# Performance work log

Hardware: AMD Instinct MI355X
Metric: run time of the kernel (lower is better)

The kernel has to match this reference:

```python
import jax, jax.numpy as jnp
import numpy as np

B, S, D, E = 8, 2048, 1024, 8
TOKENS = B * S
CAPACITY = TOKENS // E  # capacity_factor=1.0, top-1 gating (deepspeed default)


def _moe_layer(x_flat, Wg, We, be):
    """DeepSpeed-style top-1 MoE: gate -> capacity drop -> dispatch -> expert GEMM -> combine.
    x_flat: [T, D]; Wg: [D, E]; We: [E, D, D]; be: [E, D]."""
    gates = jax.nn.softmax(x_flat @ Wg, axis=-1)              # [T, E]
    idx = jnp.argmax(gates, axis=1)                            # [T] expert per token
    mask = jax.nn.one_hot(idx, E, dtype=jnp.int32)             # [T, E]
    loc = jnp.cumsum(mask, axis=0) - 1                         # position within expert
    loc_s = jnp.sum(loc * mask, axis=1)                        # [T]
    keep = loc_s < CAPACITY                                    # capacity drop
    gate_s = jnp.sum(gates * mask.astype(gates.dtype), axis=1) * keep.astype(gates.dtype)
    slot = jnp.clip(loc_s, 0, CAPACITY - 1)
    # dispatch: scatter kept tokens into [E, C, D] buffer (slots are unique for kept tokens)
    disp = jnp.zeros((E, CAPACITY, D), x_flat.dtype).at[idx, slot].add(
        x_flat * keep[:, None].astype(x_flat.dtype))
    # grouped expert GEMM
    eo = jnp.einsum('ecd,edf->ecf', disp, We) + be[:, None, :]  # [E, C, D]
    # combine: gather each token's expert output, scale by its gate value
    return eo[idx, slot] * gate_s[:, None]                      # [T, D]


def reference(x, y, W1, b1, Wg2, We2, be2, Wg3, We3, be3):
    h = jnp.einsum('bsd,df->bsf', x, W1) + b1                  # dense pre-layer
    hf = h.reshape(TOKENS, D)
    o = _moe_layer(hf, Wg2, We2, be2)
    o = _moe_layer(o, Wg3, We3, be3)
    h = h + o.reshape(B, S, D)                                 # residual add
    sent = h.mean(axis=1)                                      # [B, D]
    logp = jax.nn.log_softmax(sent, axis=-1)
    return -jnp.mean(logp[jnp.arange(B), y])                   # CrossEntropyLoss


def setup_inputs() -> dict:
    key = jax.random.key(0)
    ks = jax.random.split(key, 10)
    s = 0.02
    return {
        'x': jax.random.normal(ks[0], (B, S, D), jnp.float32),
        'y': jax.random.randint(ks[1], (B,), 0, D),
        'W1': jax.random.normal(ks[2], (D, D), jnp.float32) * s,
        'b1': jnp.zeros((D,), jnp.float32),
        'Wg2': jax.random.normal(ks[3], (D, E), jnp.float32) * s,
        'We2': jax.random.normal(ks[4], (E, D, D), jnp.float32) * s,
        'be2': jnp.zeros((E, D), jnp.float32),
        'Wg3': jax.random.normal(ks[5], (D, E), jnp.float32) * s,
        'We3': jax.random.normal(ks[6], (E, D, D), jnp.float32) * s,
        'be3': jnp.zeros((E, D), jnp.float32),
    }
```

## Files before the change

### kernel.cpp

```cpp
#include <hip/hip_runtime.h>
#include <hip/hip_bf16.h>
#include <math.h>


#define TOKS 16384
#define DIM 1024
#define NEXP 8
#define CAP 2048
#define BATCH 8
#define SEQ 2048

typedef __bf16 bf16_t;
typedef __bf16 bf16x8 __attribute__((ext_vector_type(8)));
typedef float fx4 __attribute__((ext_vector_type(4)));

__device__ __forceinline__ void gll16(const bf16_t* g, bf16_t* l) {
  __builtin_amdgcn_global_load_lds(
      (const __attribute__((address_space(1))) unsigned int*)g,
      (__attribute__((address_space(3))) unsigned int*)l, 16, 0, 0);
}

#define BARRIER() asm volatile("s_barrier" ::: "memory")
#define LGKM0()   asm volatile("s_waitcnt lgkmcnt(0)" ::: "memory")
#define VMC(N)    asm volatile("s_waitcnt vmcnt(" #N ")" ::: "memory")

#define PW_BLOCKS (17 * 64)
__global__ __launch_bounds__(256) void k_prep_w(
    const float* __restrict__ W1, const float* __restrict__ We2,
    const float* __restrict__ We3, bf16_t* __restrict__ Wt) {
  __shared__ bf16_t T[256][68];
  const int id = blockIdx.x;
  const int tid = threadIdx.x;
  const int m = id >> 6, rem = id & 63;
  const int k0 = (rem >> 4) * 256, n0 = (rem & 15) * 64;
  const float* src = (m == 0) ? W1
                     : (m <= 8) ? We2 + (size_t)(m - 1) * DIM * DIM
                                : We3 + (size_t)(m - 9) * DIM * DIM;
  bf16_t* dst = Wt + (size_t)m * DIM * DIM;
  const int r = tid >> 4, nq = tid & 15;
#pragma unroll
  for (int i = 0; i < 16; i++) {
    const int k = i * 16 + r;
    float4 v = *(const float4*)&src[(size_t)(k0 + k) * DIM + n0 + nq * 4];
    union { bf16_t h[4]; uint2 u; } t;
    t.h[0] = (bf16_t)v.x; t.h[1] = (bf16_t)v.y;
    t.h[2] = (bf16_t)v.z; t.h[3] = (bf16_t)v.w;
    *(uint2*)&T[k][(nq ^ ((k >> 3) & 15)) << 2] = t.u;
  }
  __syncthreads();
#pragma unroll
  for (int p = 0; p < 8; p++) {
    const int idx2 = p * 256 + tid;
    const int nl = idx2 >> 5, ks = (idx2 & 31) * 8;
    union { bf16_t h[8]; uint4 u; } o;
#pragma unroll
    for (int j = 0; j < 8; j++) {
      const int k = ks + j;
      o.h[j] = T[k][((((nl >> 2) ^ ((k >> 3) & 15)) << 2) | (nl & 3))];
    }
    *(uint4*)&dst[(size_t)(n0 + nl) * DIM + k0 + ks] = o.u;
  }
}

#define CVT_BLOCKS (TOKS * DIM / 8 / 256)
#define PREPX_GRID (2 + CVT_BLOCKS + 1)
__global__ __launch_bounds__(256) void k_prep_x(
    const float* __restrict__ Wg2, const float* __restrict__ Wg3,
    const float* __restrict__ x, bf16_t* __restrict__ WgP,
    bf16_t* __restrict__ xb, uint4* __restrict__ zreg, int znq) {
  const int id = blockIdx.x;
  const int tid = threadIdx.x;
  if (id < 2) {
    const int which = id;
    const float* src = which ? Wg3 : Wg2;
    bf16_t* dst = WgP + which * (128 * 8 * 8);
#pragma unroll
    for (int j = 0; j < 4; j++) {
      int d = tid * 4 + j;
      float4 a = *(const float4*)&src[d * 8];
      float4 b = *(const float4*)&src[d * 8 + 4];
      float v[8] = {a.x, a.y, a.z, a.w, b.x, b.y, b.z, b.w};
#pragma unroll
      for (int e = 0; e < 8; e++)
        dst[((d >> 3) * 8 + e) * 8 + (d & 7)] = (bf16_t)v[e];
    }
  } else if (id < 2 + CVT_BLOCKS) {
    const int cid = id - 2;
    size_t i = ((size_t)cid * 256 + tid) * 8;
    float4 a = *(const float4*)&x[i];
    float4 b = *(const float4*)&x[i + 4];
    union { bf16_t h[8]; uint4 u; } t;
    t.h[0] = (bf16_t)a.x; t.h[1] = (bf16_t)a.y; t.h[2] = (bf16_t)a.z; t.h[3] = (bf16_t)a.w;
    t.h[4] = (bf16_t)b.x; t.h[5] = (bf16_t)b.y; t.h[6] = (bf16_t)b.z; t.h[7] = (bf16_t)b.w;
    *(uint4*)&xb[i] = t.u;
  } else {
    const uint4 z = {0u, 0u, 0u, 0u};
    for (int i = tid; i < znq; i += 256) zreg[i] = z;
  }
}

template <int MODE>
__global__ __launch_bounds__(512) void k_gemm256(
    const bf16_t* __restrict__ A, const bf16_t* __restrict__ Bt0,
    const float* __restrict__ bias0, bf16_t* __restrict__ out,
    float* __restrict__ sent, const int* __restrict__ tok,
    const int* __restrict__ cnt, const float* __restrict__ gate,
    const bf16_t* __restrict__ zp, float* __restrict__ slabs) {
  __shared__ alignas(16) bf16_t As[2][256 * 64];
  __shared__ alignas(16) bf16_t Bs[2][256 * 64];
  const int tid = threadIdx.x;
  const int lane = tid & 63, wave = tid >> 6;
  const int quad = lane >> 4, l15 = lane & 15;
  const int wm = wave >> 2, wn = wave & 3;
  const int id = blockIdx.x;
  const int xcd = id & 7, rem = id >> 3;
  const int n0 = (rem & 3) * 256;

  int m0;
  int count = 0;
  const bf16_t* Bt;
  const float* bias;
  const int* tk = nullptr;
  if constexpr (MODE == 0) {
    m0 = (xcd * 8 + (rem >> 2)) * 256;
    Bt = Bt0;
    bias = bias0;
  } else {
    m0 = (rem >> 2) * 256;
    count = cnt[xcd];
    if (m0 >= count) {
      if constexpr (MODE == 2) {
        float* slab = slabs + (size_t)id * 2048;
        for (int i = tid; i < 2048; i += 512) slab[i] = 0.f;
      }
      return;
    }
    Bt = Bt0 + (size_t)xcd * DIM * DIM;
    bias = bias0 + xcd * DIM;
    tk = tok + xcd * CAP;
  }

  const int kc = (tid & 7) ^ ((tid >> 3) & 7);
  const int rbase = tid >> 3;

  const bf16_t* gA[4];
  const bf16_t* gB[4];
#pragma unroll
  for (int h = 0; h < 2; h++)
#pragma unroll
    for (int i = 0; i < 2; i++) {
      const int r = h * 128 + i * 64 + rbase;
      if constexpr (MODE == 0) {
        gA[h * 2 + i] = A + (size_t)(m0 + r) * DIM + kc * 8;
      } else {
        const int ca = m0 + r;
        gA[h * 2 + i] = (ca < count) ? A + (size_t)tk[ca] * DIM + kc * 8 : zp;
      }
      gB[h * 2 + i] = Bt + (size_t)(n0 + r) * DIM + kc * 8;
    }

  auto stA = [&](int t, int half) {
#pragma unroll
    for (int i = 0; i < 2; i++)
      gll16(gA[half * 2 + i] + t * 64,
            &As[t & 1][(half * 128 + i * 64 + wave * 8) * 64]);
  };
  auto stB = [&](int t, int half) {
#pragma unroll
    for (int i = 0; i < 2; i++)
      gll16(gB[half * 2 + i] + t * 64,
            &Bs[t & 1][(half * 128 + i * 64 + wave * 8) * 64]);
  };
  auto rdA = [&](bf16x8 (&av)[4][2], int buf, int mh) {
#pragma unroll
    for (int mf = 0; mf < 4; mf++)
#pragma unroll
      for (int s = 0; s < 2; s++)
        av[mf][s] = *(const bf16x8*)&As[buf][(wm * 128 + (mh * 4 + mf) * 16 + l15) * 64 +
                                            (((s * 4 + quad) ^ (l15 & 7)) << 3)];
  };
  auto rdB = [&](bf16x8 (&bv)[2][2], int buf, int nh) {
#pragma unroll
    for (int nf = 0; nf < 2; nf++)
#pragma unroll
      for (int s = 0; s < 2; s++)
        bv[nf][s] = *(const bf16x8*)&Bs[buf][(wn * 64 + (nh * 2 + nf) * 16 + l15) * 64 +
                                            (((s * 4 + quad) ^ (l15 & 7)) << 3)];
  };

  fx4 acc[8][4];
#pragma unroll
  for (int i = 0; i < 8; i++)
#pragma unroll
    for (int j = 0; j < 4; j++) acc[i][j] = (fx4)0.0f;

  auto mma = [&](bf16x8 (&av)[4][2], bf16x8 (&bv)[2][2], int mh, int nh) {
    __builtin_amdgcn_s_setprio(1);
#pragma unroll
    for (int s = 0; s < 2; s++)
#pragma unroll
      for (int mf = 0; mf < 4; mf++)
#pragma unroll
        for (int nf = 0; nf < 2; nf++)
          acc[mh * 4 + mf][nh * 2 + nf] = __builtin_amdgcn_mfma_f32_16x16x32_bf16(
              av[mf][s], bv[nf][s], acc[mh * 4 + mf][nh * 2 + nf], 0, 0, 0);
    __builtin_amdgcn_s_setprio(0);
  };

  stA(0, 0); stA(0, 1); stB(0, 0); stB(0, 1);
  stB(1, 0); stB(1, 1); stA(1, 0);
  VMC(6);
  BARRIER();

  bf16x8 av0[4][2], av1[4][2], bv0[2][2], bv1[2][2];
#pragma unroll 2
  for (int t = 0; t < 14; t++) {
    const int buf = t & 1;
    rdA(av0, buf, 0); rdB(bv0, buf, 0); rdB(bv1, buf, 1);
    stA(t + 1, 1);
    BARRIER(); LGKM0();
    mma(av0, bv0, 0, 0);
    BARRIER();
    stB(t + 2, 0);
    BARRIER();
    mma(av0, bv1, 0, 1);
    BARRIER();
    rdA(av1, buf, 1);
    stB(t + 2, 1);
    BARRIER(); LGKM0();
    mma(av1, bv1, 1, 1);
    BARRIER();
    stA(t + 2, 0);
    mma(av1, bv0, 1, 0);
    VMC(6);
    BARRIER();
  }
  {
    rdA(av0, 0, 0); rdB(bv0, 0, 0); rdB(bv1, 0, 1);
    stA(15, 1);
    BARRIER(); LGKM0();
    mma(av0, bv0, 0, 0);
    BARRIER();
    mma(av0, bv1, 0, 1);
    BARRIER();
    rdA(av1, 0, 1);
    BARRIER(); LGKM0();
    mma(av1, bv1, 1, 1);
    BARRIER();
    mma(av1, bv0, 1, 0);
    VMC(0);
    BARRIER();
  }
  {
    rdA(av0, 1, 0); rdB(bv0, 1, 0); rdB(bv1, 1, 1); rdA(av1, 1, 1);
    LGKM0();
    mma(av0, bv0, 0, 0); mma(av0, bv1, 0, 1);
    mma(av1, bv1, 1, 1); mma(av1, bv0, 1, 0);
  }

  float bb[4];
#pragma unroll
  for (int nf = 0; nf < 4; nf++) bb[nf] = bias[n0 + wn * 64 + nf * 16 + l15];
  if constexpr (MODE == 0) {
    float sj[4] = {0.f, 0.f, 0.f, 0.f};
#pragma unroll
    for (int mf = 0; mf < 8; mf++)
#pragma unroll
      for (int r = 0; r < 4; r++) {
        const int rowL = wm * 128 + mf * 16 + quad * 4 + r;
#pragma unroll
        for (int nf = 0; nf < 4; nf++) {
          const float v = acc[mf][nf][r] + bb[nf];
          sj[nf] += v;
          out[(size_t)(m0 + rowL) * DIM + n0 + wn * 64 + nf * 16 + l15] = (bf16_t)v;
        }
      }
#pragma unroll
    for (int nf = 0; nf < 4; nf++) {
      sj[nf] += __shfl_xor(sj[nf], 16);
      sj[nf] += __shfl_xor(sj[nf], 32);
    }
    if (quad == 0)
#pragma unroll
      for (int nf = 0; nf < 4; nf++)
        atomicAdd(&sent[(m0 >> 11) * DIM + n0 + wn * 64 + nf * 16 + l15],
                  sj[nf] * (1.0f / SEQ));
  } else if constexpr (MODE == 1) {
#pragma unroll
    for (int mf = 0; mf < 8; mf++)
#pragma unroll
      for (int r = 0; r < 4; r++) {
        const int c = m0 + wm * 128 + mf * 16 + quad * 4 + r;
        if (c < count) {
          const int tkn = tk[c];
          const float g = gate[tkn];
#pragma unroll
          for (int nf = 0; nf < 4; nf++)
            out[(size_t)tkn * DIM + n0 + wn * 64 + nf * 16 + l15] =
                (bf16_t)((acc[mf][nf][r] + bb[nf]) * g);
        }
      }
  } else {
    float colacc[4][8];
#pragma unroll
    for (int nf = 0; nf < 4; nf++)
#pragma unroll
      for (int b2 = 0; b2 < 8; b2++) colacc[nf][b2] = 0.f;
#pragma unroll
    for (int mf = 0; mf < 8; mf++)
#pragma unroll
      for (int r = 0; r < 4; r++) {
        const int c = m0 + wm * 128 + mf * 16 + quad * 4 + r;
        if (c < count) {
          const int tkn = tk[c];
          const float g = gate[tkn];
          const int b = tkn >> 11;
#pragma unroll
          for (int nf = 0; nf < 4; nf++) {
            const float v = (acc[mf][nf][r] + bb[nf]) * g;
#pragma unroll
            for (int b2 = 0; b2 < 8; b2++)
              colacc[nf][b2] += (b == b2) ? v : 0.f;
          }
        }
      }
#pragma unroll
    for (int nf = 0; nf < 4; nf++)
#pragma unroll
      for (int b2 = 0; b2 < 8; b2++) {
        colacc[nf][b2] += __shfl_xor(colacc[nf][b2], 16);
        colacc[nf][b2] += __shfl_xor(colacc[nf][b2], 32);
      }
    __syncthreads();
    float* swm = (float*)&As[0][0];
    if (quad == 0) {
#pragma unroll
      for (int nf = 0; nf < 4; nf++)
#pragma unroll
        for (int b2 = 0; b2 < 8; b2++)
          swm[(wm * 8 + b2) * 256 + wn * 64 + nf * 16 + l15] = colacc[nf][b2];
    }
    __syncthreads();
    float* slab = slabs + (size_t)id * 2048;
    for (int i = tid; i < 2048; i += 512)
      slab[i] = swm[i] + swm[2048 + i];
  }
}

__global__ __launch_bounds__(256) void k_gate_mm(
    const bf16_t* __restrict__ act, const bf16_t* __restrict__ WgPx,
    int* __restrict__ idx, float* __restrict__ gate) {
  __shared__ alignas(16) bf16_t As[64 * 64];
  __shared__ alignas(16) bf16_t WgS[128 * 64];
  __shared__ float L[64][8];
  const int tid = threadIdx.x;
  const int lane = tid & 63, wave = tid >> 6;
  const int quad = lane >> 4, l15 = lane & 15;
  const int m0 = blockIdx.x * 64;
  const int kc = (tid & 7) ^ ((tid >> 3) & 7);
  const int rbase = tid >> 3;

#pragma unroll
  for (int j = 0; j < 4; j++)
    gll16(WgPx + (j * 256 + wave * 64 + lane) * 8, &WgS[(j * 256 + wave * 64) * 8]);

  const bf16_t* gA[2]; bf16_t* lA[2];
#pragma unroll
  for (int i = 0; i < 2; i++) {
    gA[i] = act + (size_t)(m0 + rbase + 32 * i) * DIM + kc * 8;
    lA[i] = &As[wave * 512 + i * 2048];
  }
  fx4 acc = (fx4)0.0f;
  for (int k0 = 0; k0 < DIM; k0 += 64) {
#pragma unroll
    for (int i = 0; i < 2; i++) gll16(gA[i] + k0, lA[i]);
    __syncthreads();
#pragma unroll
    for (int s = 0; s < 2; s++) {
      const int pofs = ((s * 4 + quad) ^ (l15 & 7)) << 3;
      bf16x8 av = *(const bf16x8*)&As[(wave * 16 + l15) * 64 + pofs];
      bf16x8 bv = *(const bf16x8*)&WgS[((k0 >> 3) + s * 4 + quad) * 64 + (l15 & 7) * 8];
      acc = __builtin_amdgcn_mfma_f32_16x16x32_bf16(av, bv, acc, 0, 0, 0);
    }
    __syncthreads();
  }
  if (l15 < 8) {
#pragma unroll
    for (int r = 0; r < 4; r++) L[wave * 16 + quad * 4 + r][l15] = acc[r];
  }
  __syncthreads();
  if (tid < 64) {
    float lg[8];
#pragma unroll
    for (int e = 0; e < 8; e++) lg[e] = L[tid][e];
    float best = lg[0];
    int bi = 0;
#pragma unroll
    for (int e = 1; e < 8; e++)
      if (lg[e] > best) { best = lg[e]; bi = e; }
    float s = 0.f;
#pragma unroll
    for (int e = 0; e < 8; e++) s += expf(lg[e] - best);
    idx[m0 + tid] = bi;
    gate[m0 + tid] = 1.0f / s;
  }
}

#define DLMAX 2048
__global__ __launch_bounds__(1024) void k_route(
    const int* __restrict__ idx, int* __restrict__ tok, int* __restrict__ cnt,
    bf16_t* __restrict__ obuf) {
  const int e = blockIdx.x;
  const int tid = threadIdx.x, lane = tid & 63, wv = tid >> 6;
  __shared__ int wsum[16];
  __shared__ int dlist[DLMAX];
  const int4* p = (const int4*)(idx + tid * 16);
  int m[16];
  int c = 0;
#pragma unroll
  for (int j = 0; j < 4; j++) {
    int4 v = p[j];
    m[j * 4 + 0] = (v.x == e);
    m[j * 4 + 1] = (v.y == e);
    m[j * 4 + 2] = (v.z == e);
    m[j * 4 + 3] = (v.w == e);
    c += m[j * 4] + m[j * 4 + 1] + m[j * 4 + 2] + m[j * 4 + 3];
  }
  int sc = c;
#pragma unroll
  for (int off = 1; off < 64; off <<= 1) {
    int n = __shfl_up(sc, off);
    if (lane >= off) sc += n;
  }
  if (lane == 63) wsum[wv] = sc;
  __syncthreads();
  int wb = 0, tot = 0;
#pragma unroll
  for (int i = 0; i < 16; i++) {
    int s = wsum[i];
    tot += s;
    if (i < wv) wb += s;
  }
  int pos = wb + sc - c;
  const uint4 z = {0u, 0u, 0u, 0u};
#pragma unroll
  for (int j = 0; j < 16; j++) {
    if (m[j]) {
      int t = tid * 16 + j;
      if (pos < CAP) {
        tok[e * CAP + pos] = t;
      } else {
        int di = pos - CAP;
        if (di < DLMAX) dlist[di] = t;
        else
          for (int k = 0; k < 128; k++) *(uint4*)&obuf[(size_t)t * DIM + k * 8] = z;
      }
      pos++;
    }
  }
  if (tid == 0) cnt[e] = tot < CAP ? tot : CAP;
  __syncthreads();
  int ndl = tot - CAP;
  ndl = ndl < 0 ? 0 : (ndl > DLMAX ? DLMAX : ndl);
  for (int d = tid >> 7; d < ndl; d += 8) {
    int t = dlist[d];
    *(uint4*)&obuf[(size_t)t * DIM + (tid & 127) * 8] = z;
  }
}

__global__ __launch_bounds__(256) void k_sum(
    const float* __restrict__ slabs, const float* __restrict__ sent,
    float* __restrict__ sentF) {
  const int b = blockIdx.x >> 2, sub = blockIdx.x & 3;
  const int tid = threadIdx.x;
  float a = 0.f;
#pragma unroll 1
  for (int rg = 0; rg < 8; rg++) {
    const int rem = rg * 4 + sub;
#pragma unroll
    for (int xcd = 0; xcd < 8; xcd++)
      a += slabs[(size_t)(rem * 8 + xcd) * 2048 + b * 256 + tid];
  }
  const int col = sub * 256 + tid;
  sentF[b * DIM + col] = sent[b * DIM + col] + a * (1.0f / SEQ);
}

__global__ __launch_bounds__(256) void k_loss(
    const float* __restrict__ sentF, const int* __restrict__ y,
    float* __restrict__ out) {
  const int tid = threadIdx.x;
  __shared__ float red[256];
  float total = 0.f;
  for (int b = 0; b < BATCH; b++) {
    const int c4 = tid * 4;
    float4 f = *(const float4*)&sentF[b * DIM + c4];
    float m = fmaxf(fmaxf(f.x, f.y), fmaxf(f.z, f.w));
    red[tid] = m;
    __syncthreads();
    for (int s = 128; s; s >>= 1) {
      if (tid < s) red[tid] = fmaxf(red[tid], red[tid + s]);
      __syncthreads();
    }
    m = red[0];
    __syncthreads();
    float sum = expf(f.x - m) + expf(f.y - m) + expf(f.z - m) + expf(f.w - m);
    red[tid] = sum;
    __syncthreads();
    for (int s = 128; s; s >>= 1) {
      if (tid < s) red[tid] += red[tid + s];
      __syncthreads();
    }
    if (tid == 0) total += m + logf(red[0]) - sentF[b * DIM + y[b]];
    __syncthreads();
  }
  if (tid == 0) out[0] = total * (1.0f / BATCH);
}

extern "C" void kernel_launch(void* const* d_in, const int* in_sizes, int n_in,
                              void* d_out, int out_size, void* d_ws, size_t ws_size,
                              hipStream_t stream) {
  (void)in_sizes; (void)n_in; (void)out_size; (void)ws_size;
  const float* x   = (const float*)d_in[0];
  const int*   y   = (const int*)d_in[1];
  const float* W1  = (const float*)d_in[2];
  const float* b1  = (const float*)d_in[3];
  const float* Wg2 = (const float*)d_in[4];
  const float* We2 = (const float*)d_in[5];
  const float* be2 = (const float*)d_in[6];
  const float* Wg3 = (const float*)d_in[7];
  const float* We3 = (const float*)d_in[8];
  const float* be3 = (const float*)d_in[9];

  char* p = (char*)d_ws;
  size_t off = 0;
  auto carve = [&](size_t bytes) -> char* {
    char* r = p + off;
    off += (bytes + 255) & ~(size_t)255;
    return r;
  };
  bf16_t* Wt   = (bf16_t*)carve((size_t)17 * DIM * DIM * 2);
  bf16_t* WgP  = (bf16_t*)carve(2 * 128 * 8 * 8 * 2);
  bf16_t* h    = (bf16_t*)carve((size_t)TOKS * DIM * 2);
  bf16_t* o1   = (bf16_t*)carve((size_t)TOKS * DIM * 2);
  bf16_t* o2   = (bf16_t*)carve((size_t)TOKS * DIM * 2);
  int*    idx  = (int*)carve(TOKS * 4);
  float*  gate = (float*)carve(TOKS * 4);
  int*    tok  = (int*)carve(NEXP * CAP * 4);
  int*    cnt  = (int*)carve(NEXP * 4);
  size_t zoff0 = off;
  float*  sent = (float*)carve(BATCH * DIM * 4);
  bf16_t* zp   = (bf16_t*)carve(4096);
  size_t zbytes = off - zoff0;
  float*  slabs = (float*)carve((size_t)256 * 2048 * 4);
  float*  sentF = (float*)carve((size_t)BATCH * DIM * 4);
  bf16_t* xb   = o2;

  k_prep_w<<<PW_BLOCKS, 256, 0, stream>>>(W1, We2, We3, Wt);
  k_prep_x<<<PREPX_GRID, 256, 0, stream>>>(
      Wg2, Wg3, x, WgP, xb, (uint4*)sent, (int)(zbytes / 16));

  k_gemm256<0><<<256, 512, 0, stream>>>(
      xb, Wt, b1, h, sent, nullptr, nullptr, nullptr, zp, nullptr);

  k_gate_mm<<<TOKS / 64, 256, 0, stream>>>(h, WgP, idx, gate);
  k_route<<<NEXP, 1024, 0, stream>>>(idx, tok, cnt, o1);
  k_gemm256<1><<<256, 512, 0, stream>>>(
      h, Wt + (size_t)1 * DIM * DIM, be2, o1, nullptr, tok, cnt, gate, zp, nullptr);

  k_gate_mm<<<TOKS / 64, 256, 0, stream>>>(o1, WgP + 128 * 8 * 8, idx, gate);
  k_route<<<NEXP, 1024, 0, stream>>>(idx, tok, cnt, o2);
  k_gemm256<2><<<256, 512, 0, stream>>>(
      o1, Wt + (size_t)9 * DIM * DIM, be3, nullptr, nullptr, tok, cnt, gate, zp, slabs);

  k_sum<<<32, 256, 0, stream>>>(slabs, sent, sentF);
  k_loss<<<1, 256, 0, stream>>>(sentF, y, (float*)d_out);
}
```

Baseline: 351.8 us.

## Restructure GEMM main loop prefetch schedule with manual two-stage unroll

Reorders the global-to-LDS prefetch issue in the expert GEMM mainloop. B is now prefetched two stages ahead and A one stage ahead, with the loads spread across the four MFMA sub-blocks. The loop is manually unrolled by two with constant buffer indices, and vmcnt waits drop to 4. The goal is to balance memory issue against MFMA work and cut stalls. It adds a tighter dependency on LDS buffer reuse timing, which risks races or extra waits.

Result: no change. 358.3 us (+1.8%).

```diff
diff --git a/kernel.cpp b/kernel.cpp
--- a/kernel.cpp
+++ b/kernel.cpp
@@ -207,40 +207,63 @@
     __builtin_amdgcn_s_setprio(0);
   };
 
-  stA(0, 0); stA(0, 1); stB(0, 0); stB(0, 1);
-  stB(1, 0); stB(1, 1); stA(1, 0);
-  VMC(6);
+  stB(0, 0); stB(0, 1); stA(0, 0); stA(0, 1);
+  stB(1, 0); stB(1, 1);
+  VMC(4);
   BARRIER();
 
   bf16x8 av0[4][2], av1[4][2], bv0[2][2], bv1[2][2];
-#pragma unroll 2
-  for (int t = 0; t < 14; t++) {
-    const int buf = t & 1;
-    rdA(av0, buf, 0); rdB(bv0, buf, 0); rdB(bv1, buf, 1);
-    stA(t + 1, 1);
+#pragma unroll 1
+  for (int i = 0; i < 7; i++) {
+    const int t0 = 2 * i;
+    rdA(av0, 0, 0); rdB(bv0, 0, 0);
+    stA(t0 + 1, 0);
     BARRIER(); LGKM0();
     mma(av0, bv0, 0, 0);
     BARRIER();
-    stB(t + 2, 0);
-    BARRIER();
+    rdB(bv1, 0, 1);
+    stA(t0 + 1, 1);
+    BARRIER(); LGKM0();
     mma(av0, bv1, 0, 1);
     BARRIER();
-    rdA(av1, buf, 1);
-    stB(t + 2, 1);
+    rdA(av1, 0, 1);
+    stB(t0 + 2, 0);
     BARRIER(); LGKM0();
     mma(av1, bv1, 1, 1);
     BARRIER();
-    stA(t + 2, 0);
+    stB(t0 + 2, 1);
     mma(av1, bv0, 1, 0);
-    VMC(6);
+    VMC(4);
+    BARRIER();
+    rdA(av0, 1, 0); rdB(bv0, 1, 0);
+    stA(t0 + 2, 0);
+    BARRIER(); LGKM0();
+    mma(av0, bv0, 0, 0);
+    BARRIER();
+    rdB(bv1, 1, 1);
+    stA(t0 + 2, 1);
+    BARRIER(); LGKM0();
+    mma(av0, bv1, 0, 1);
+    BARRIER();
+    rdA(av1, 1, 1);
+    stB(t0 + 3, 0);
+    BARRIER(); LGKM0();
+    mma(av1, bv1, 1, 1);
+    BARRIER();
+    stB(t0 + 3, 1);
+    mma(av1, bv0, 1, 0);
+    VMC(4);
     BARRIER();
   }
   {
-    rdA(av0, 0, 0); rdB(bv0, 0, 0); rdB(bv1, 0, 1);
+    rdA(av0, 0, 0); rdB(bv0, 0, 0);
+    stA(15, 0);
+    BARRIER(); LGKM0();
+    mma(av0, bv0, 0, 0);
+    BARRIER();
+    rdB(bv1, 0, 1);
     stA(15, 1);
     BARRIER(); LGKM0();
-    mma(av0, bv0, 0, 0);
-    BARRIER();
     mma(av0, bv1, 0, 1);
     BARRIER();
     rdA(av1, 0, 1);
@@ -250,8 +273,6 @@
     mma(av1, bv0, 1, 0);
     VMC(0);
     BARRIER();
-  }
-  {
     rdA(av0, 1, 0); rdB(bv0, 1, 0); rdB(bv1, 1, 1); rdA(av1, 1, 1);
     LGKM0();
     mma(av0, bv0, 0, 0); mma(av0, bv1, 0, 1);
```
